# Kernel tuning notes

Hardware: AMD Instinct MI355X
Metric: run time of the kernel (lower is better)

The kernel has to match this reference:

```python
import jax, jax.numpy as jnp
import numpy as np

NUM_HEADS = 16
ROPE_BASE = 10000.0


def _rope_cos_sin(seq_len, head_dim, dtype):
    inv_freq = 1.0 / (ROPE_BASE ** (jnp.arange(0, head_dim, 2, dtype=jnp.float32) / head_dim))
    t = jnp.arange(seq_len, dtype=jnp.float32)
    freqs = jnp.einsum('i,j->ij', t, inv_freq)          # [S, hd/2]
    emb = jnp.concatenate([freqs, freqs], axis=-1)      # [S, hd]
    return jnp.cos(emb).astype(dtype), jnp.sin(emb).astype(dtype)


def _rotate_half(x):
    x1, x2 = jnp.split(x, 2, axis=-1)
    return jnp.concatenate([-x2, x1], axis=-1)


def setup_inputs() -> dict:
    key = jax.random.key(0)
    k1, k2, k3 = jax.random.split(key, 3)
    B, S, D = 2, 2048, 2048
    x = jax.random.normal(k1, (B, S, D), dtype=jnp.float32)
    w_qkv = jax.random.normal(k2, (D, 3 * D), dtype=jnp.float32) * (D ** -0.5)
    w_out = jax.random.normal(k3, (D, D), dtype=jnp.float32) * (D ** -0.5)
    return {"x": x, "w_qkv": w_qkv, "w_out": w_out}


def reference(x, w_qkv, w_out):
    B, S, D = x.shape
    H = NUM_HEADS
    hd = D // H
    scale = hd ** -0.5

    qkv = jnp.einsum('bsd,de->bse', x, w_qkv)            # [B,S,3D]
    q, k, v = jnp.split(qkv, 3, axis=-1)
    # -> [B,H,S,hd]
    q = q.reshape(B, S, H, hd).transpose(0, 2, 1, 3)
    k = k.reshape(B, S, H, hd).transpose(0, 2, 1, 3)
    v = v.reshape(B, S, H, hd).transpose(0, 2, 1, 3)

    cos, sin = _rope_cos_sin(S, hd, x.dtype)             # [S,hd]
    cos = cos[None, None]                                # [1,1,S,hd]
    sin = sin[None, None]
    q = q * cos + _rotate_half(q) * sin
    k = k * cos + _rotate_half(k) * sin

    scores = jnp.einsum('bhqd,bhkd->bhqk', q, k) * scale  # [B,H,S,S]
    attn = jax.nn.softmax(scores, axis=-1)                # non-causal: no mask
    out = jnp.einsum('bhqk,bhkd->bhqd', attn, v)          # [B,H,S,hd]
    out = out.transpose(0, 2, 1, 3).reshape(B, S, D)
    out = jnp.einsum('bsd,de->bse', out, w_out)
    return out
```

## Files before the change

### kernel.cpp

```cpp
#include <hip/hip_runtime.h>
#include <hip/hip_bf16.h>

typedef __hip_bfloat16 bf16_t;
typedef __bf16 bf16x8 __attribute__((ext_vector_type(8)));
typedef float floatx4 __attribute__((ext_vector_type(4)));

#define DEVINL __device__ __forceinline__

DEVINL floatx4 mfma16(bf16x8 a, bf16x8 b, floatx4 c) {
  return __builtin_amdgcn_mfma_f32_16x16x32_bf16(a, b, c, 0, 0, 0);
}

DEVINL void gload_lds16(const bf16_t* gp, bf16_t* lp) {
  __builtin_amdgcn_global_load_lds(
      (const __attribute__((address_space(1))) unsigned int*)gp,
      (__attribute__((address_space(3))) unsigned int*)lp, 16, 0, 0);
}

template <class CT> DEVINL CT cvtC(float f);
template <> DEVINL bf16_t cvtC<bf16_t>(float f) { return __float2bfloat16(f); }
template <> DEVINL float cvtC<float>(float f) { return f; }

DEVINL unsigned int pack_bf2(float a, float b) {
  union { bf16_t h; unsigned short s; } ua, ub;
  ua.h = __float2bfloat16(a);
  ub.h = __float2bfloat16(b);
  return (unsigned int)ua.s | ((unsigned int)ub.s << 16);
}

__global__ void convert_f32_bf16(const float* __restrict__ in,
                                 bf16_t* __restrict__ out) {
  size_t i = ((size_t)blockIdx.x * 256 + threadIdx.x) * 8;
  floatx4 a = *(const floatx4*)(in + i);
  floatx4 b = *(const floatx4*)(in + i + 4);
  bf16x8 r;
#pragma unroll
  for (int j = 0; j < 4; j++) r[j] = (__bf16)a[j];
#pragma unroll
  for (int j = 0; j < 4; j++) r[4 + j] = (__bf16)b[j];
  *(bf16x8*)(out + i) = r;
}

template <class CT>
__global__ __launch_bounds__(256, 2) void gemm_bt(
    const bf16_t* __restrict__ A, const bf16_t* __restrict__ BT,
    CT* __restrict__ C, int M, int N, int K) {
  __shared__ __align__(16) bf16_t a_lds[8 * 1024];
  __shared__ __align__(16) bf16_t b_lds[8 * 1024];

  const int tid = threadIdx.x;
  const int wave = tid >> 6;
  const int lane = tid & 63;
  const int quad = lane >> 4;
  const int l16 = lane & 15;
  const int wm = wave >> 1, wn = wave & 1;

  const int row0 = blockIdx.y * 128;
  const int col0 = blockIdx.x * 128;

  floatx4 acc[4][4] = {};

  const bf16_t* ag = A + (size_t)(row0 + wave * 32 + l16) * K + quad * 8;
  const bf16_t* bg = BT + (size_t)(col0 + wave * 32 + l16) * K + quad * 8;

  for (int k0 = 0; k0 < K; k0 += 64) {
#pragma unroll
    for (int t = 0; t < 2; t++) {
      bf16_t* al = a_lds + (wave * 2 + t) * 1024;
      bf16_t* bl = b_lds + (wave * 2 + t) * 1024;
      const bf16_t* agt = ag + k0 + (size_t)(t * 16) * K;
      const bf16_t* bgt = bg + k0 + (size_t)(t * 16) * K;
#pragma unroll
      for (int kc = 0; kc < 2; kc++) {
        gload_lds16(agt + kc * 32, al + kc * 512);
        gload_lds16(bgt + kc * 32, bl + kc * 512);
      }
    }
    __syncthreads();
#pragma unroll
    for (int kc = 0; kc < 2; kc++) {
      bf16x8 af[4], bfr[4];
#pragma unroll
      for (int i = 0; i < 4; i++)
        af[i] = *(const bf16x8*)(a_lds + (wm * 4 + i) * 1024 + kc * 512 +
                                 lane * 8);
#pragma unroll
      for (int j = 0; j < 4; j++)
        bfr[j] = *(const bf16x8*)(b_lds + (wn * 4 + j) * 1024 + kc * 512 +
                                  lane * 8);
#pragma unroll
      for (int i = 0; i < 4; i++)
#pragma unroll
        for (int j = 0; j < 4; j++)
          acc[i][j] = mfma16(af[i], bfr[j], acc[i][j]);
    }
    __syncthreads();
  }

#pragma unroll
  for (int i = 0; i < 4; i++)
#pragma unroll
    for (int j = 0; j < 4; j++)
#pragma unroll
      for (int r = 0; r < 4; r++) {
        int row = row0 + wm * 64 + i * 16 + quad * 4 + r;
        int col = col0 + wn * 64 + j * 16 + l16;
        C[(size_t)row * N + col] = cvtC<CT>(acc[i][j][r]);
      }
}

__global__ void transposecvt(const float* __restrict__ in,
                             bf16_t* __restrict__ out, int M, int N) {
  __shared__ bf16_t tile[32][33];
  int n0 = blockIdx.x * 32, m0 = blockIdx.y * 32;
  tile[threadIdx.y][threadIdx.x] =
      __float2bfloat16(in[(size_t)(m0 + threadIdx.y) * N + n0 + threadIdx.x]);
  __syncthreads();
  out[(size_t)(n0 + threadIdx.y) * M + m0 + threadIdx.x] =
      tile[threadIdx.x][threadIdx.y];
}

__global__ void transpose_v(const bf16_t* __restrict__ qkv,
                            bf16_t* __restrict__ VT) {
  __shared__ bf16_t tile[32][33];
  int bh = blockIdx.z;
  int b = bh >> 4, h = bh & 15;
  int s0 = blockIdx.x * 32, d0 = blockIdx.y * 32;
  tile[threadIdx.y][threadIdx.x] =
      qkv[(((size_t)(b * 2048 + s0 + threadIdx.y) * 3) + 2) * 2048 + h * 128 +
          d0 + threadIdx.x];
  __syncthreads();
  VT[((size_t)bh * 128 + d0 + threadIdx.y) * 2048 + s0 + threadIdx.x] =
      tile[threadIdx.x][threadIdx.y];
}

__global__ void rope_qk(bf16_t* __restrict__ qkv) {
  struct __align__(8) bf4 { bf16_t v[4]; };
  int t = blockIdx.x * 256 + threadIdx.x;
  int dc = t & 15;
  int s = (t >> 4) & 2047;
  int h = (t >> 15) & 15;
  int b = t >> 19;
  int d = dc * 4;
  size_t base = ((size_t)(b * 2048 + s) * 3) * 2048 + h * 128;
  bf4 ql = *(const bf4*)(qkv + base + d);
  bf4 qh = *(const bf4*)(qkv + base + d + 64);
  bf4 kl = *(const bf4*)(qkv + base + 2048 + d);
  bf4 kh = *(const bf4*)(qkv + base + 2048 + d + 64);
  bf4 oql, oqh, okl, okh;
  const float scale = 0.08838834764831845f;
#pragma unroll
  for (int i = 0; i < 4; i++) {
    int j = d + i;
    float fr = (float)s * powf(10000.0f, -(float)j * (1.0f / 64.0f));
    float c = cosf(fr);
    float sn = sinf(fr);
    float qlo = __bfloat162float(ql.v[i]), qhi = __bfloat162float(qh.v[i]);
    float klo = __bfloat162float(kl.v[i]), khi = __bfloat162float(kh.v[i]);
    oql.v[i] = __float2bfloat16((qlo * c - qhi * sn) * scale);
    oqh.v[i] = __float2bfloat16((qhi * c + qlo * sn) * scale);
    okl.v[i] = __float2bfloat16(klo * c - khi * sn);
    okh.v[i] = __float2bfloat16(khi * c + klo * sn);
  }
  *(bf4*)(qkv + base + d) = oql;
  *(bf4*)(qkv + base + d + 64) = oqh;
  *(bf4*)(qkv + base + 2048 + d) = okl;
  *(bf4*)(qkv + base + 2048 + d + 64) = okh;
}

__global__ __launch_bounds__(256, 2) void flash_attn(
    const bf16_t* __restrict__ qkv, const bf16_t* __restrict__ VT,
    bf16_t* __restrict__ Out) {
  const int S = 2048;
  const int RS = 6144;
  const int tid = threadIdx.x;
  const int wave = tid >> 6;
  const int lane = tid & 63;
  const int quad = lane >> 4;
  const int l16 = lane & 15;

  const int bh = blockIdx.y;
  const int q0 = blockIdx.x * 128;
  const int b = bh >> 4, h = bh & 15;

  const bf16_t* Qb = qkv + (size_t)b * S * RS + h * 128;
  const bf16_t* Kb = Qb + 2048;
  const bf16_t* Vb = VT + (size_t)bh * 128 * S;

  __shared__ __align__(16) bf16_t k_lds[16384];
  __shared__ __align__(16) bf16_t v_lds[16384];

  bf16x8 qf[2][4];
#pragma unroll
  for (int qn = 0; qn < 2; qn++)
#pragma unroll
    for (int ks = 0; ks < 4; ks++)
      qf[qn][ks] = *(const bf16x8*)(
          Qb + (size_t)(q0 + wave * 32 + qn * 16 + l16) * RS + ks * 32 +
          quad * 8);

  floatx4 o_acc[2][8] = {};
  float l_part[2] = {0.f, 0.f};

  const int sA = l16 + 32 * (quad & 1);
  const int sB = sA + 16;
  const bool hi = quad >= 2;

  for (int kt = 0; kt < S / 128; kt++) {
    const int kk0 = kt * 128;
#pragma unroll
    for (int t = 0; t < 2; t++) {
      int mt = wave * 2 + t;
#pragma unroll
      for (int ks = 0; ks < 4; ks++) {
        gload_lds16(Kb + (size_t)(kk0 + mt * 16 + l16) * RS + ks * 32 + quad * 8,
                    k_lds + mt * 2048 + ks * 512);
        gload_lds16(Vb + (size_t)(mt * 16 + l16) * S + kk0 + ks * 32 + quad * 8,
                    v_lds + mt * 2048 + ks * 512);
      }
    }
    __syncthreads();

    floatx4 s_acc[2][8] = {};
#pragma unroll
    for (int ks = 0; ks < 4; ks++)
#pragma unroll
      for (int mt = 0; mt < 8; mt++) {
        bf16x8 kf = *(const bf16x8*)(k_lds + mt * 2048 + ks * 512 + lane * 8);
        s_acc[0][mt] = mfma16(kf, qf[0][ks], s_acc[0][mt]);
        s_acc[1][mt] = mfma16(kf, qf[1][ks], s_acc[1][mt]);
      }

    unsigned int p01[2][8], p23[2][8];
#pragma unroll
    for (int qn = 0; qn < 2; qn++)
#pragma unroll
      for (int mt = 0; mt < 8; mt++) {
        float e0 = __expf(s_acc[qn][mt][0]);
        float e1 = __expf(s_acc[qn][mt][1]);
        float e2 = __expf(s_acc[qn][mt][2]);
        float e3 = __expf(s_acc[qn][mt][3]);
        l_part[qn] += (e0 + e1) + (e2 + e3);
        p01[qn][mt] = pack_bf2(e0, e1);
        p23[qn][mt] = pack_bf2(e2, e3);
      }

#pragma unroll
    for (int kc = 0; kc < 4; kc++) {
#pragma unroll
      for (int qn = 0; qn < 2; qn++) {
        unsigned int a0 = __shfl(p01[qn][2 * kc], sA);
        unsigned int b0 = __shfl(p01[qn][2 * kc + 1], sA);
        unsigned int a1 = __shfl(p23[qn][2 * kc], sA);
        unsigned int b1 = __shfl(p23[qn][2 * kc + 1], sA);
        unsigned int a2 = __shfl(p01[qn][2 * kc], sB);
        unsigned int b2 = __shfl(p01[qn][2 * kc + 1], sB);
        unsigned int a3 = __shfl(p23[qn][2 * kc], sB);
        unsigned int b3 = __shfl(p23[qn][2 * kc + 1], sB);
        union { unsigned int u[4]; bf16x8 v; } bp;
        bp.u[0] = hi ? b0 : a0;
        bp.u[1] = hi ? b1 : a1;
        bp.u[2] = hi ? b2 : a2;
        bp.u[3] = hi ? b3 : a3;
#pragma unroll
        for (int dt = 0; dt < 8; dt++) {
          bf16x8 vf = *(const bf16x8*)(v_lds + dt * 2048 + kc * 512 + lane * 8);
          o_acc[qn][dt] = mfma16(vf, bp.v, o_acc[qn][dt]);
        }
      }
    }
    __syncthreads();
  }

#pragma unroll
  for (int qn = 0; qn < 2; qn++) {
    l_part[qn] += __shfl_xor(l_part[qn], 16);
    l_part[qn] += __shfl_xor(l_part[qn], 32);
  }

  struct __align__(8) bf4 { bf16_t v[4]; };
#pragma unroll
  for (int qn = 0; qn < 2; qn++) {
    float inv = 1.f / l_part[qn];
    size_t s = q0 + wave * 32 + qn * 16 + l16;
#pragma unroll
    for (int dt = 0; dt < 8; dt++) {
      bf4 o;
#pragma unroll
      for (int r = 0; r < 4; r++)
        o.v[r] = __float2bfloat16(o_acc[qn][dt][r] * inv);
      *(bf4*)(Out + ((size_t)b * S + s) * 2048 + h * 128 + dt * 16 + quad * 4) = o;
    }
  }
}

extern "C" void kernel_launch(void* const* d_in, const int* in_sizes, int n_in,
                              void* d_out, int out_size, void* d_ws,
                              size_t ws_size, hipStream_t stream) {
  const float* x = (const float*)d_in[0];
  const float* w_qkv = (const float*)d_in[1];
  const float* w_out = (const float*)d_in[2];
  float* out = (float*)d_out;
  char* ws = (char*)d_ws;

  const int B = 2, S = 2048, D = 2048;
  bf16_t* qkv = (bf16_t*)(ws);
  bf16_t* wqkvT = (bf16_t*)(ws + (size_t)B * S * 3 * D * 2);
  bf16_t* xbf = (bf16_t*)(ws + (size_t)B * S * 3 * D * 2 + (size_t)3 * D * D * 2);
  bf16_t* VT = xbf;
  bf16_t* attn = wqkvT;
  bf16_t* woutT = qkv;

  dim3 b32(32, 32);
  convert_f32_bf16<<<(B * S * D) / 2048, 256, 0, stream>>>(x, xbf);
  transposecvt<<<dim3(3 * D / 32, D / 32), b32, 0, stream>>>(w_qkv, wqkvT, D, 3 * D);
  gemm_bt<bf16_t><<<dim3(3 * D / 128, B * S / 128), 256, 0, stream>>>(
      xbf, wqkvT, qkv, B * S, 3 * D, D);
  rope_qk<<<4096, 256, 0, stream>>>(qkv);
  transpose_v<<<dim3(S / 32, 4, B * 16), b32, 0, stream>>>(qkv, VT);
  flash_attn<<<dim3(S / 128, B * 16), 256, 0, stream>>>(qkv, VT, attn);
  transposecvt<<<dim3(D / 32, D / 32), b32, 0, stream>>>(w_out, woutT, D, D);
  gemm_bt<float><<<dim3(D / 128, B * S / 128), 256, 0, stream>>>(
      attn, woutT, out, B * S, D, D);
}
```

Measured before the change: 531.4 us.

## Fuse V transpose into QKV GEMM epilogue, register-prefetch tiles, swizzle blocks

The QKV GEMM epilogue now writes the V columns straight into the transposed VT layout, which removes the separate transpose_v kernel and shrinks the qkv buffer to Q and K only. The GEMM main loop swaps direct global-to-LDS loads for register prefetch of the next K tile, overlapping global loads with MFMA work at the cost of an extra barrier per iteration. The launch becomes a 1D grid with grouped block ordering for L2 reuse, and occupancy is raised to 3 blocks per SM. Rope and flash attention strides are updated to the narrower row layout.

```diff
diff --git a/kernel.cpp b/kernel.cpp
--- a/kernel.cpp
+++ b/kernel.cpp
@@ -41,10 +41,11 @@
   *(bf16x8*)(out + i) = r;
 }
 
-template <class CT>
-__global__ __launch_bounds__(256, 2) void gemm_bt(
+template <bool SPLITV, class CT>
+__global__ __launch_bounds__(256, 3) void gemm_bt(
     const bf16_t* __restrict__ A, const bf16_t* __restrict__ BT,
-    CT* __restrict__ C, int M, int N, int K) {
+    CT* __restrict__ C, bf16_t* __restrict__ VTout, int M, int N, int CN,
+    int K) {
   __shared__ __align__(16) bf16_t a_lds[8 * 1024];
   __shared__ __align__(16) bf16_t b_lds[8 * 1024];
 
@@ -55,28 +56,43 @@
   const int l16 = lane & 15;
   const int wm = wave >> 1, wn = wave & 1;
 
-  const int row0 = blockIdx.y * 128;
-  const int col0 = blockIdx.x * 128;
+  const int nx = N >> 7;
+  const int bid = blockIdx.x;
+  const int row0 = ((bid & 7) + 8 * (bid / (8 * nx))) * 128;
+  const int col0 = ((bid >> 3) % nx) * 128;
 
   floatx4 acc[4][4] = {};
 
   const bf16_t* ag = A + (size_t)(row0 + wave * 32 + l16) * K + quad * 8;
   const bf16_t* bg = BT + (size_t)(col0 + wave * 32 + l16) * K + quad * 8;
 
+  bf16x8 pa[2][2], pb[2][2];
+#define LOAD_TILE(k0)                                                       \
+  {                                                                         \
+    _Pragma("unroll") for (int t = 0; t < 2; t++)                           \
+        _Pragma("unroll") for (int kc = 0; kc < 2; kc++) {                  \
+      pa[t][kc] = *(const bf16x8*)(ag + (k0) + (size_t)(t * 16) * K + kc * 32); \
+      pb[t][kc] = *(const bf16x8*)(bg + (k0) + (size_t)(t * 16) * K + kc * 32); \
+    }                                                                       \
+  }
+#define STORE_TILE()                                                        \
+  {                                                                         \
+    _Pragma("unroll") for (int t = 0; t < 2; t++)                           \
+        _Pragma("unroll") for (int kc = 0; kc < 2; kc++) {                  \
+      *(bf16x8*)(a_lds + (wave * 2 + t) * 1024 + kc * 512 + lane * 8) =     \
+          pa[t][kc];                                                        \
+      *(bf16x8*)(b_lds + (wave * 2 + t) * 1024 + kc * 512 + lane * 8) =     \
+          pb[t][kc];                                                        \
+    }                                                                       \
+  }
+
+  LOAD_TILE(0);
+  STORE_TILE();
+  __syncthreads();
+
   for (int k0 = 0; k0 < K; k0 += 64) {
-#pragma unroll
-    for (int t = 0; t < 2; t++) {
-      bf16_t* al = a_lds + (wave * 2 + t) * 1024;
-      bf16_t* bl = b_lds + (wave * 2 + t) * 1024;
-      const bf16_t* agt = ag + k0 + (size_t)(t * 16) * K;
-      const bf16_t* bgt = bg + k0 + (size_t)(t * 16) * K;
-#pragma unroll
-      for (int kc = 0; kc < 2; kc++) {
-        gload_lds16(agt + kc * 32, al + kc * 512);
-        gload_lds16(bgt + kc * 32, bl + kc * 512);
-      }
-    }
-    __syncthreads();
+    const bool more = (k0 + 64) < K;
+    if (more) LOAD_TILE(k0 + 64);
 #pragma unroll
     for (int kc = 0; kc < 2; kc++) {
       bf16x8 af[4], bfr[4];
@@ -95,18 +111,41 @@
           acc[i][j] = mfma16(af[i], bfr[j], acc[i][j]);
     }
     __syncthreads();
-  }
-
-#pragma unroll
-  for (int i = 0; i < 4; i++)
-#pragma unroll
-    for (int j = 0; j < 4; j++)
-#pragma unroll
-      for (int r = 0; r < 4; r++) {
-        int row = row0 + wm * 64 + i * 16 + quad * 4 + r;
-        int col = col0 + wn * 64 + j * 16 + l16;
-        C[(size_t)row * N + col] = cvtC<CT>(acc[i][j][r]);
-      }
+    if (more) STORE_TILE();
+    __syncthreads();
+  }
+#undef LOAD_TILE
+#undef STORE_TILE
+
+  if (!SPLITV || col0 < 4096) {
+#pragma unroll
+    for (int i = 0; i < 4; i++)
+#pragma unroll
+      for (int j = 0; j < 4; j++)
+#pragma unroll
+        for (int r = 0; r < 4; r++) {
+          int row = row0 + wm * 64 + i * 16 + quad * 4 + r;
+          int col = col0 + wn * 64 + j * 16 + l16;
+          C[(size_t)row * CN + col] = cvtC<CT>(acc[i][j][r]);
+        }
+  } else {
+    const int h = (col0 - 4096) >> 7;
+    const int b = row0 >> 11;
+    const int s0 = row0 & 2047;
+    bf16_t* vt = VTout + (size_t)(b * 16 + h) * 128 * 2048;
+    struct __align__(8) bf4 { bf16_t v[4]; };
+#pragma unroll
+    for (int i = 0; i < 4; i++)
+#pragma unroll
+      for (int j = 0; j < 4; j++) {
+        int d = wn * 64 + j * 16 + l16;
+        int s = s0 + wm * 64 + i * 16 + quad * 4;
+        bf4 o;
+#pragma unroll
+        for (int r = 0; r < 4; r++) o.v[r] = __float2bfloat16(acc[i][j][r]);
+        *(bf4*)(vt + (size_t)d * 2048 + s) = o;
+      }
+  }
 }
 
 __global__ void transposecvt(const float* __restrict__ in,
@@ -120,20 +159,6 @@
       tile[threadIdx.x][threadIdx.y];
 }
 
-__global__ void transpose_v(const bf16_t* __restrict__ qkv,
-                            bf16_t* __restrict__ VT) {
-  __shared__ bf16_t tile[32][33];
-  int bh = blockIdx.z;
-  int b = bh >> 4, h = bh & 15;
-  int s0 = blockIdx.x * 32, d0 = blockIdx.y * 32;
-  tile[threadIdx.y][threadIdx.x] =
-      qkv[(((size_t)(b * 2048 + s0 + threadIdx.y) * 3) + 2) * 2048 + h * 128 +
-          d0 + threadIdx.x];
-  __syncthreads();
-  VT[((size_t)bh * 128 + d0 + threadIdx.y) * 2048 + s0 + threadIdx.x] =
-      tile[threadIdx.x][threadIdx.y];
-}
-
 __global__ void rope_qk(bf16_t* __restrict__ qkv) {
   struct __align__(8) bf4 { bf16_t v[4]; };
   int t = blockIdx.x * 256 + threadIdx.x;
@@ -142,7 +167,7 @@
   int h = (t >> 15) & 15;
   int b = t >> 19;
   int d = dc * 4;
-  size_t base = ((size_t)(b * 2048 + s) * 3) * 2048 + h * 128;
+  size_t base = ((size_t)(b * 2048 + s) * 2) * 2048 + h * 128;
   bf4 ql = *(const bf4*)(qkv + base + d);
   bf4 qh = *(const bf4*)(qkv + base + d + 64);
   bf4 kl = *(const bf4*)(qkv + base + 2048 + d);
@@ -172,7 +197,7 @@
     const bf16_t* __restrict__ qkv, const bf16_t* __restrict__ VT,
     bf16_t* __restrict__ Out) {
   const int S = 2048;
-  const int RS = 6144;
+  const int RS = 4096;
   const int tid = threadIdx.x;
   const int wave = tid >> 6;
   const int lane = tid & 63;
@@ -304,22 +329,22 @@
   char* ws = (char*)d_ws;
 
   const int B = 2, S = 2048, D = 2048;
-  bf16_t* qkv = (bf16_t*)(ws);
-  bf16_t* wqkvT = (bf16_t*)(ws + (size_t)B * S * 3 * D * 2);
-  bf16_t* xbf = (bf16_t*)(ws + (size_t)B * S * 3 * D * 2 + (size_t)3 * D * D * 2);
-  bf16_t* VT = xbf;
+  bf16_t* qkv2 = (bf16_t*)(ws);
+  bf16_t* wqkvT = (bf16_t*)(ws + (size_t)B * S * 2 * D * 2);
+  bf16_t* xbf = (bf16_t*)(ws + (size_t)B * S * 2 * D * 2 + (size_t)3 * D * D * 2);
+  bf16_t* VT = (bf16_t*)(ws + (size_t)B * S * 2 * D * 2 + (size_t)3 * D * D * 2 +
+                         (size_t)B * S * D * 2);
   bf16_t* attn = wqkvT;
-  bf16_t* woutT = qkv;
+  bf16_t* woutT = qkv2;
 
   dim3 b32(32, 32);
   convert_f32_bf16<<<(B * S * D) / 2048, 256, 0, stream>>>(x, xbf);
   transposecvt<<<dim3(3 * D / 32, D / 32), b32, 0, stream>>>(w_qkv, wqkvT, D, 3 * D);
-  gemm_bt<bf16_t><<<dim3(3 * D / 128, B * S / 128), 256, 0, stream>>>(
-      xbf, wqkvT, qkv, B * S, 3 * D, D);
-  rope_qk<<<4096, 256, 0, stream>>>(qkv);
-  transpose_v<<<dim3(S / 32, 4, B * 16), b32, 0, stream>>>(qkv, VT);
-  flash_attn<<<dim3(S / 128, B * 16), 256, 0, stream>>>(qkv, VT, attn);
+  gemm_bt<true, bf16_t><<<(B * S / 128) * (3 * D / 128), 256, 0, stream>>>(
+      xbf, wqkvT, qkv2, VT, B * S, 3 * D, 2 * D, D);
+  rope_qk<<<4096, 256, 0, stream>>>(qkv2);
+  flash_attn<<<dim3(S / 128, B * 16), 256, 0, stream>>>(qkv2, VT, attn);
   transposecvt<<<dim3(D / 32, D / 32), b32, 0, stream>>>(w_out, woutT, D, D);
-  gemm_bt<float><<<dim3(D / 128, B * S / 128), 256, 0, stream>>>(
-      attn, woutT, out, B * S, D, D);
-}
+  gemm_bt<false, float><<<(B * S / 128) * (D / 128), 256, 0, stream>>>(
+      attn, woutT, out, nullptr, B * S, D, D, D);
+}
```

Measured after the change: 521.1 us. Within noise of the previous version (-1.9%).
